# Optimization experiments

Hardware: AMD Instinct MI355X
Metric: run time of the kernel (lower is better)

Reference implementation:

```python
import jax, jax.numpy as jnp
import numpy as np

THRESHOLD = 0.5
EPS_STD = 1e-08
EPS_DEG = 1e-08


def setup_inputs() -> dict:
    key = jax.random.key(0)
    x = jax.random.normal(key, (32, 64, 1000, 16), dtype=jnp.float32)
    return {"x": x}


def reference(x):
    # x: [B, C, T, F]
    B, C, T, F = x.shape
    # permute(0,1,3,2).reshape(B, C, F*T)
    xr = jnp.transpose(x, (0, 1, 3, 2)).reshape(B, C, F * T)
    mean = jnp.mean(xr, axis=2, keepdims=True)
    # torch.std is unbiased (ddof=1)
    std = jnp.std(xr, axis=2, keepdims=True, ddof=1) + EPS_STD
    xn = (xr - mean) / std
    # [B, C, C] correlation-style adjacency (note: divided by T, as in source)
    adj = jnp.einsum('bcd,bed->bce', xn, xn) / T
    adj = (adj > THRESHOLD).astype(x.dtype)
    adj = adj + jnp.eye(C, dtype=x.dtype)[None, :, :]
    degree = jnp.sum(adj, axis=2, keepdims=True)            # [B, C, 1]
    dsi = (degree + EPS_DEG) ** -0.5
    adj = adj * dsi * jnp.transpose(dsi, (0, 2, 1))          # D^-1/2 A D^-1/2
    return adj
```

## Files before the change

kernel.cpp:

```cpp
#include <hip/hip_runtime.h>

#define B_SZ 32
#define C_CH 64
#define D_TOT 16000
#define N_CHUNK 25
#define CHUNK 640
#define KT 128
#define NT 5

typedef short bf16x8 __attribute__((ext_vector_type(8)));
typedef short short4v __attribute__((ext_vector_type(4)));
typedef float f32x4 __attribute__((ext_vector_type(4)));

#define WS_G_ELEMS (B_SZ * C_CH * C_CH)
#define WS_S_ELEMS (B_SZ * C_CH)

__device__ __forceinline__ short f2bf(float f) {
    unsigned u = __builtin_bit_cast(unsigned, f);
    u = (u + 0x7FFFu + ((u >> 16) & 1u)) >> 16;
    return (short)u;
}

__global__ __launch_bounds__(256) void gram_mfma(
    const float* __restrict__ x, float* __restrict__ wsG, float* __restrict__ wsS)
{
    __shared__ __align__(16) short tile[2][C_CH * KT];

    const int t = threadIdx.x;
    const int b = blockIdx.y;
    const int chunk = blockIdx.x;
    const int l = t & 63;
    const int w = t >> 6;
    const int w0 = (w >> 1) * 32;
    const int w1 = (w & 1) * 32;

    const float* xb = x + (size_t)b * (C_CH * D_TOT) + chunk * CHUNK;

    const int lch = t >> 5;
    const int ldp = (t & 31) * 4;
    const float* rp[8];
    int wb[8];
    #pragma unroll
    for (int j = 0; j < 8; ++j) {
        const int ch = lch + 8 * j;
        rp[j] = xb + (size_t)ch * D_TOT + ldp;
        wb[j] = (ch * 256 + ldp * 2) ^ ((ch & 7) << 4);
    }

    const int fl = l & 15;
    const int fg = (l >> 4) * 16;

    f32x4 acc[2][2];
    #pragma unroll
    for (int i = 0; i < 2; ++i)
        #pragma unroll
        for (int k = 0; k < 2; ++k)
            acc[i][k] = (f32x4){0.f, 0.f, 0.f, 0.f};

    float ssum[8];
    #pragma unroll
    for (int j = 0; j < 8; ++j) ssum[j] = 0.f;

    float4 ld[8];

    #pragma unroll
    for (int j = 0; j < 8; ++j) ld[j] = *reinterpret_cast<const float4*>(rp[j]);
    {
        char* buf = (char*)tile[0];
        #pragma unroll
        for (int j = 0; j < 8; ++j) {
            const float4 v = ld[j];
            ssum[j] += v.x + v.y + v.z + v.w;
            short4v s;
            s[0] = f2bf(v.x); s[1] = f2bf(v.y); s[2] = f2bf(v.z); s[3] = f2bf(v.w);
            *reinterpret_cast<short4v*>(buf + wb[j]) = s;
        }
    }
    __syncthreads();

    #pragma unroll
    for (int tt = 0; tt < NT; ++tt) {
        if (tt + 1 < NT) {
            #pragma unroll
            for (int j = 0; j < 8; ++j)
                ld[j] = *reinterpret_cast<const float4*>(rp[j] + (tt + 1) * KT);
        }

        {
            const char* buf = (const char*)tile[tt & 1];
            #pragma unroll
            for (int kk = 0; kk < 4; ++kk) {
                const int k64 = kk * 64;
                const int chA0 = w0 + fl,      chA1 = w0 + 16 + fl;
                const int chB0 = w1 + fl,      chB1 = w1 + 16 + fl;
                const bf16x8 a0 = *reinterpret_cast<const bf16x8*>(
                    buf + ((chA0 * 256 + fg + k64) ^ ((chA0 & 7) << 4)));
                const bf16x8 a1 = *reinterpret_cast<const bf16x8*>(
                    buf + ((chA1 * 256 + fg + k64) ^ ((chA1 & 7) << 4)));
                const bf16x8 b0 = *reinterpret_cast<const bf16x8*>(
                    buf + ((chB0 * 256 + fg + k64) ^ ((chB0 & 7) << 4)));
                const bf16x8 b1 = *reinterpret_cast<const bf16x8*>(
                    buf + ((chB1 * 256 + fg + k64) ^ ((chB1 & 7) << 4)));
                acc[0][0] = __builtin_amdgcn_mfma_f32_16x16x32_bf16(a0, b0, acc[0][0], 0, 0, 0);
                acc[0][1] = __builtin_amdgcn_mfma_f32_16x16x32_bf16(a0, b1, acc[0][1], 0, 0, 0);
                acc[1][0] = __builtin_amdgcn_mfma_f32_16x16x32_bf16(a1, b0, acc[1][0], 0, 0, 0);
                acc[1][1] = __builtin_amdgcn_mfma_f32_16x16x32_bf16(a1, b1, acc[1][1], 0, 0, 0);
            }
        }

        if (tt + 1 < NT) {
            char* buf = (char*)tile[(tt + 1) & 1];
            #pragma unroll
            for (int j = 0; j < 8; ++j) {
                const float4 v = ld[j];
                ssum[j] += v.x + v.y + v.z + v.w;
                short4v s;
                s[0] = f2bf(v.x); s[1] = f2bf(v.y); s[2] = f2bf(v.z); s[3] = f2bf(v.w);
                *reinterpret_cast<short4v*>(buf + wb[j]) = s;
            }
        }
        __syncthreads();
    }

    #pragma unroll
    for (int j = 0; j < 8; ++j) {
        float v = ssum[j];
        v += __shfl_xor(v, 1);
        v += __shfl_xor(v, 2);
        v += __shfl_xor(v, 4);
        v += __shfl_xor(v, 8);
        v += __shfl_xor(v, 16);
        if ((t & 31) == 0) atomicAdd(&wsS[b * C_CH + lch + 8 * j], v);
    }

    float* gOut = wsG + (size_t)b * (C_CH * C_CH);
    const int crow = w0 + ((l >> 4) << 2);
    const int ccol = w1 + fl;
    #pragma unroll
    for (int ct = 0; ct < 2; ++ct)
        #pragma unroll
        for (int tj = 0; tj < 2; ++tj)
            #pragma unroll
            for (int r = 0; r < 4; ++r)
                atomicAdd(&gOut[(crow + ct * 16 + r) * 64 + (ccol + tj * 16)],
                          acc[ct][tj][r]);
}

__global__ __launch_bounds__(256) void finalize_kernel(
    const float* __restrict__ wsG, const float* __restrict__ wsS, float* __restrict__ out)
{
    __shared__ float shS[64];
    __shared__ float shStd[64];
    __shared__ float shDeg[64];
    __shared__ float shDsi[64];
    __shared__ float shBin[64][65];
    const int b = blockIdx.x;
    const int t = threadIdx.x;
    const float* G = wsG + (size_t)b * (C_CH * C_CH);

    if (t < 64) {
        const float S = wsS[b * C_CH + t];
        const float gcc = G[t * 64 + t];
        const float mean = S * (1.0f / 16000.0f);
        const float var = (gcc - S * mean) * (1.0f / 15999.0f);
        shS[t] = S;
        shStd[t] = sqrtf(var) + 1e-8f;
    }
    __syncthreads();

    const int r  = t >> 2;
    const int cb = (t & 3) * 16;
    const float Sc = shS[r];
    const float stdc = shStd[r];
    float deg = 0.0f;
    #pragma unroll
    for (int m = 0; m < 16; ++m) {
        const int e = cb + m;
        const float g = G[r * 64 + e];
        const float a = (g - Sc * shS[e] * (1.0f / 16000.0f)) / (stdc * shStd[e] * 1000.0f);
        float bin = (a > 0.5f) ? 1.0f : 0.0f;
        if (e == r) bin += 1.0f;
        shBin[r][e] = bin;
        deg += bin;
    }
    deg += __shfl_xor(deg, 1);
    deg += __shfl_xor(deg, 2);
    if ((t & 3) == 0) shDeg[r] = deg;
    __syncthreads();
    if (t < 64) shDsi[t] = 1.0f / sqrtf(shDeg[t] + 1e-8f);
    __syncthreads();

    float* ob = out + (size_t)b * (C_CH * C_CH);
    const float dr = shDsi[r];
    #pragma unroll
    for (int m = 0; m < 16; ++m) {
        const int e = cb + m;
        ob[r * 64 + e] = shBin[r][e] * dr * shDsi[e];
    }
}

extern "C" void kernel_launch(void* const* d_in, const int* in_sizes, int n_in,
                              void* d_out, int out_size, void* d_ws, size_t ws_size,
                              hipStream_t stream)
{
    const float* x = (const float*)d_in[0];
    float* out = (float*)d_out;
    float* wsG = (float*)d_ws;
    float* wsS = (float*)d_ws + WS_G_ELEMS;

    hipMemsetAsync(d_ws, 0, (WS_G_ELEMS + WS_S_ELEMS) * sizeof(float), stream);
    gram_mfma<<<dim3(N_CHUNK, B_SZ), 256, 0, stream>>>(x, wsG, wsS);
    finalize_kernel<<<B_SZ, 256, 0, stream>>>(wsG, wsS, out);
}
```

Before: 199.6 us.

## Replace atomic Gram accumulation with partial buffers and a separate reduction kernel

Each chunk block now writes its partial Gram matrix and channel sums to dedicated slots instead of using atomicAdd into a zeroed workspace. This removes the memset and the atomic contention, and a new reduce_g kernel sums the 25 partials. The load pipeline is also restructured to prefetch two tiles ahead and convert before the MFMA loop, with paired bf16 packing. The cost is an extra kernel launch and roughly 13 MB of partial-buffer traffic.

```diff
diff --git a/kernel.cpp b/kernel.cpp
--- a/kernel.cpp
+++ b/kernel.cpp
@@ -3,26 +3,27 @@
 #define B_SZ 32
 #define C_CH 64
 #define D_TOT 16000
-#define N_CHUNK 25
+#define NP 25
 #define CHUNK 640
 #define KT 128
 #define NT 5
 
 typedef short bf16x8 __attribute__((ext_vector_type(8)));
-typedef short short4v __attribute__((ext_vector_type(4)));
 typedef float f32x4 __attribute__((ext_vector_type(4)));
 
-#define WS_G_ELEMS (B_SZ * C_CH * C_CH)
-#define WS_S_ELEMS (B_SZ * C_CH)
-
-__device__ __forceinline__ short f2bf(float f) {
-    unsigned u = __builtin_bit_cast(unsigned, f);
-    u = (u + 0x7FFFu + ((u >> 16) & 1u)) >> 16;
-    return (short)u;
+#define PARTG_ELEMS (NP * B_SZ * 4096)
+#define PARTS_ELEMS (NP * B_SZ * 64)
+
+__device__ __forceinline__ unsigned f2bf_pk(float a, float b) {
+    unsigned ua = __builtin_bit_cast(unsigned, a);
+    unsigned ub = __builtin_bit_cast(unsigned, b);
+    ua = (ua + 0x7FFFu + ((ua >> 16) & 1u)) >> 16;
+    ub = (ub + 0x7FFFu + ((ub >> 16) & 1u)) >> 16;
+    return (ua & 0xFFFFu) | (ub << 16);
 }
 
 __global__ __launch_bounds__(256) void gram_mfma(
-    const float* __restrict__ x, float* __restrict__ wsG, float* __restrict__ wsS)
+    const float* __restrict__ x, float* __restrict__ partG, float* __restrict__ partS)
 {
     __shared__ __align__(16) short tile[2][C_CH * KT];
 
@@ -63,29 +64,37 @@
 
     float4 ld[8];
 
+#define CVT_STORE(BUFIDX)                                                        \
+    {                                                                            \
+        char* buf_ = (char*)tile[BUFIDX];                                        \
+        _Pragma("unroll")                                                        \
+        for (int j = 0; j < 8; ++j) {                                            \
+            const float4 v = ld[j];                                              \
+            ssum[j] += v.x + v.y + v.z + v.w;                                    \
+            uint2 u;                                                             \
+            u.x = f2bf_pk(v.x, v.y);                                             \
+            u.y = f2bf_pk(v.z, v.w);                                             \
+            *reinterpret_cast<uint2*>(buf_ + wb[j]) = u;                         \
+        }                                                                        \
+    }
+
     #pragma unroll
     for (int j = 0; j < 8; ++j) ld[j] = *reinterpret_cast<const float4*>(rp[j]);
-    {
-        char* buf = (char*)tile[0];
-        #pragma unroll
-        for (int j = 0; j < 8; ++j) {
-            const float4 v = ld[j];
-            ssum[j] += v.x + v.y + v.z + v.w;
-            short4v s;
-            s[0] = f2bf(v.x); s[1] = f2bf(v.y); s[2] = f2bf(v.z); s[3] = f2bf(v.w);
-            *reinterpret_cast<short4v*>(buf + wb[j]) = s;
-        }
-    }
+    CVT_STORE(0)
+    #pragma unroll
+    for (int j = 0; j < 8; ++j) ld[j] = *reinterpret_cast<const float4*>(rp[j] + KT);
     __syncthreads();
 
     #pragma unroll
     for (int tt = 0; tt < NT; ++tt) {
         if (tt + 1 < NT) {
-            #pragma unroll
-            for (int j = 0; j < 8; ++j)
-                ld[j] = *reinterpret_cast<const float4*>(rp[j] + (tt + 1) * KT);
+            CVT_STORE((tt + 1) & 1)
+            if (tt + 2 < NT) {
+                #pragma unroll
+                for (int j = 0; j < 8; ++j)
+                    ld[j] = *reinterpret_cast<const float4*>(rp[j] + (tt + 2) * KT);
+            }
         }
-
         {
             const char* buf = (const char*)tile[tt & 1];
             #pragma unroll
@@ -107,21 +116,11 @@
                 acc[1][1] = __builtin_amdgcn_mfma_f32_16x16x32_bf16(a1, b1, acc[1][1], 0, 0, 0);
             }
         }
-
-        if (tt + 1 < NT) {
-            char* buf = (char*)tile[(tt + 1) & 1];
-            #pragma unroll
-            for (int j = 0; j < 8; ++j) {
-                const float4 v = ld[j];
-                ssum[j] += v.x + v.y + v.z + v.w;
-                short4v s;
-                s[0] = f2bf(v.x); s[1] = f2bf(v.y); s[2] = f2bf(v.z); s[3] = f2bf(v.w);
-                *reinterpret_cast<short4v*>(buf + wb[j]) = s;
-            }
-        }
         __syncthreads();
     }
-
+#undef CVT_STORE
+
+    const size_t pbase = (size_t)(chunk * B_SZ + b);
     #pragma unroll
     for (int j = 0; j < 8; ++j) {
         float v = ssum[j];
@@ -130,10 +129,10 @@
         v += __shfl_xor(v, 4);
         v += __shfl_xor(v, 8);
         v += __shfl_xor(v, 16);
-        if ((t & 31) == 0) atomicAdd(&wsS[b * C_CH + lch + 8 * j], v);
-    }
-
-    float* gOut = wsG + (size_t)b * (C_CH * C_CH);
+        if ((t & 31) == 0) partS[pbase * 64 + lch + 8 * j] = v;
+    }
+
+    float* gOut = partG + pbase * 4096;
     const int crow = w0 + ((l >> 4) << 2);
     const int ccol = w1 + fl;
     #pragma unroll
@@ -142,12 +141,24 @@
         for (int tj = 0; tj < 2; ++tj)
             #pragma unroll
             for (int r = 0; r < 4; ++r)
-                atomicAdd(&gOut[(crow + ct * 16 + r) * 64 + (ccol + tj * 16)],
-                          acc[ct][tj][r]);
+                gOut[(crow + ct * 16 + r) * 64 + (ccol + tj * 16)] = acc[ct][tj][r];
+}
+
+__global__ __launch_bounds__(256) void reduce_g(
+    const float* __restrict__ partG, float* __restrict__ redG)
+{
+    const int i = blockIdx.x * 256 + threadIdx.x;
+    const int b = i >> 10;
+    const int o = (i & 1023) * 4;
+    f32x4 s = (f32x4){0.f, 0.f, 0.f, 0.f};
+    #pragma unroll
+    for (int c = 0; c < NP; ++c)
+        s += *reinterpret_cast<const f32x4*>(partG + ((size_t)(c * B_SZ + b)) * 4096 + o);
+    *reinterpret_cast<f32x4*>(redG + (size_t)b * 4096 + o) = s;
 }
 
 __global__ __launch_bounds__(256) void finalize_kernel(
-    const float* __restrict__ wsG, const float* __restrict__ wsS, float* __restrict__ out)
+    const float* __restrict__ redG, const float* __restrict__ partS, float* __restrict__ out)
 {
     __shared__ float shS[64];
     __shared__ float shStd[64];
@@ -156,10 +167,13 @@
     __shared__ float shBin[64][65];
     const int b = blockIdx.x;
     const int t = threadIdx.x;
-    const float* G = wsG + (size_t)b * (C_CH * C_CH);
+    const float* G = redG + (size_t)b * 4096;
 
     if (t < 64) {
-        const float S = wsS[b * C_CH + t];
+        float S = 0.f;
+        #pragma unroll
+        for (int c = 0; c < NP; ++c)
+            S += partS[(size_t)(c * B_SZ + b) * 64 + t];
         const float gcc = G[t * 64 + t];
         const float mean = S * (1.0f / 16000.0f);
         const float var = (gcc - S * mean) * (1.0f / 15999.0f);
@@ -190,7 +204,7 @@
     if (t < 64) shDsi[t] = 1.0f / sqrtf(shDeg[t] + 1e-8f);
     __syncthreads();
 
-    float* ob = out + (size_t)b * (C_CH * C_CH);
+    float* ob = out + (size_t)b * 4096;
     const float dr = shDsi[r];
     #pragma unroll
     for (int m = 0; m < 16; ++m) {
@@ -205,10 +219,11 @@
 {
     const float* x = (const float*)d_in[0];
     float* out = (float*)d_out;
-    float* wsG = (float*)d_ws;
-    float* wsS = (float*)d_ws + WS_G_ELEMS;
-
-    hipMemsetAsync(d_ws, 0, (WS_G_ELEMS + WS_S_ELEMS) * sizeof(float), stream);
-    gram_mfma<<<dim3(N_CHUNK, B_SZ), 256, 0, stream>>>(x, wsG, wsS);
-    finalize_kernel<<<B_SZ, 256, 0, stream>>>(wsG, wsS, out);
-}
+    float* partG = (float*)d_ws;
+    float* partS = partG + PARTG_ELEMS;
+    float* redG  = partS + PARTS_ELEMS;
+
+    gram_mfma<<<dim3(NP, B_SZ), 256, 0, stream>>>(x, partG, partS);
+    reduce_g<<<128, 256, 0, stream>>>(partG, redG);
+    finalize_kernel<<<B_SZ, 256, 0, stream>>>(redG, partS, out);
+}
```

Result: no change. 198.2 us (-0.7%).
